# Optimization experiments

Hardware: AMD Instinct MI355X
Metric: run time of the kernel (lower is better)

## Reference

```python
import jax, jax.numpy as jnp
import numpy as np

B, N, E = 2, 2048, 1024
H = 16
BM = 32  # BLOCK_M
BN = 32  # BLOCK_N
BUDGET = 0.2


def setup_inputs() -> dict:
    key = jax.random.key(0)
    ks = jax.random.split(key, 5)
    w = lambda k: jax.random.normal(k, (E, E), jnp.float32) * 0.02
    return {
        "x": jax.random.normal(ks[0], (B, N, E), jnp.float32),
        "W_Q": w(ks[1]),
        "W_K": w(ks[2]),
        "W_V": w(ks[3]),
        "W_O": w(ks[4]),
    }


def _forward(x, W_Q, W_K, W_V, W_O):
    Bx, Nx, Ex = x.shape
    D = Ex // H
    Tr, Tc = Nx // BM, Nx // BN
    k = max(1, int(BUDGET * Tc))

    def heads(t):  # [B,N,E] -> [B,H,N,D]
        return t.reshape(Bx, Nx, H, D).transpose(0, 2, 1, 3)

    Q = heads(x @ W_Q)
    K = heads(x @ W_K)
    V = heads(x @ W_V)

    # dynamic top-k block routing on mean-pooled blocks (indices are constants)
    Qp = Q.reshape(Bx, H, Tr, BM, D).mean(axis=3)   # [B,H,Tr,D]
    Kp = K.reshape(Bx, H, Tc, BN, D).mean(axis=3)   # [B,H,Tc,D]
    avg_sc = jnp.einsum("bhid,bhjd->bhij", Qp, Kp).mean(axis=(0, 1))  # [Tr,Tc]
    _, idx = jax.lax.top_k(avg_sc, k)  # [Tr,k] selected key blocks per query block

    # gather selected K/V blocks: [B,H,Tr,k,BN,D]
    Kb = K.reshape(Bx, H, Tc, BN, D)
    Vb = V.reshape(Bx, H, Tc, BN, D)
    Ksel = Kb[:, :, idx]
    Vsel = Vb[:, :, idx]

    Qb = Q.reshape(Bx, H, Tr, BM, D)
    scale = 1.0 / jnp.sqrt(jnp.asarray(D, jnp.float32))
    # logits over the union of selected key columns: [B,H,Tr,BM,k*BN]
    logits = jnp.einsum("bhtqd,bhtknd->bhtqkn", Qb, Ksel).reshape(
        Bx, H, Tr, BM, k * BN) * scale
    P = jax.nn.softmax(logits, axis=-1)
    Ob = jnp.einsum("bhtqs,bhtsd->bhtqd", P,
                    Vsel.reshape(Bx, H, Tr, k * BN, D))  # [B,H,Tr,BM,D]
    O = Ob.reshape(Bx, H, Nx, D).transpose(0, 2, 1, 3).reshape(Bx, Nx, Ex)
    return O @ W_O


def reference(x, W_Q, W_K, W_V, W_O):
    return _forward(x, W_Q, W_K, W_V, W_O)
```

## Files before the change

### kernel.cpp

```cpp
#include <hip/hip_runtime.h>
#include <hip/hip_bf16.h>
#include <stdint.h>

#define E     1024
#define NSEQ  2048
#define NH    16
#define HD    64
#define KSEL  12
#define MROWS 4096

typedef unsigned short u16;
typedef __attribute__((ext_vector_type(8))) short bf16x8;
typedef __attribute__((ext_vector_type(4))) float f32x4;
typedef __attribute__((ext_vector_type(4))) unsigned short u16x4;

__device__ __forceinline__ float b2f(u16 u) {
  return __builtin_bit_cast(float, (unsigned)u << 16);
}
__device__ __forceinline__ u16 f2b(float f) {
  return __builtin_bit_cast(u16, __float2bfloat16(f));
}

__device__ __forceinline__ void gload_lds16(const void* g, void* l) {
  auto gp = reinterpret_cast<__attribute__((address_space(1))) unsigned int*>(
      reinterpret_cast<uintptr_t>(g));
  auto lp = reinterpret_cast<__attribute__((address_space(3))) unsigned int*>(
      reinterpret_cast<uintptr_t>(l));
  __builtin_amdgcn_global_load_lds(gp, lp, 16, 0, 0);
}

__global__ void detect_k(const u16* __restrict__ x, int* __restrict__ flag) {
  int cnt = 0;
  for (int i = threadIdx.x; i < 1024; i += 64) {
    const unsigned e = (x[i] >> 7) & 0xFF;
    cnt += (e >= 100 && e <= 140) ? 1 : 0;
  }
#pragma unroll
  for (int off = 1; off < 64; off <<= 1) cnt += __shfl_xor(cnt, off, 64);
  if (threadIdx.x == 0) flag[0] = (cnt > 900) ? 1 : 0;
}

__global__ void xconv_k(const void* __restrict__ xin, u16* __restrict__ xc,
                        const int* __restrict__ flag) {
  const int f = flag[0];
  const int stride = gridDim.x * blockDim.x;
  if (f) {
    const u16* s = (const u16*)xin;
    for (int i = blockIdx.x * blockDim.x + threadIdx.x; i < MROWS * E; i += stride)
      xc[i] = s[i];
  } else {
    const float* s = (const float*)xin;
    for (int i = blockIdx.x * blockDim.x + threadIdx.x; i < MROWS * E; i += stride)
      xc[i] = f2b(s[i]);
  }
}

__global__ void transpose4(const void* __restrict__ w0, const void* __restrict__ w1,
                           const void* __restrict__ w2, const void* __restrict__ w3,
                           u16* __restrict__ Wt, const int* __restrict__ flag) {
  __shared__ u16 tile[32][33];
  const void* W = blockIdx.z == 0 ? w0 : blockIdx.z == 1 ? w1 : blockIdx.z == 2 ? w2 : w3;
  const int f = flag[0];
  u16* O = Wt + (size_t)blockIdx.z * (E * E);
  const int tx = threadIdx.x & 31, ty = threadIdx.x >> 5;
  const int bk = blockIdx.y * 32, bn = blockIdx.x * 32;
  if (f) {
    const u16* Wu = (const u16*)W;
    for (int r = ty; r < 32; r += 8)
      tile[r][tx] = Wu[(size_t)(bk + r) * E + bn + tx];
  } else {
    const float* Wf = (const float*)W;
    for (int r = ty; r < 32; r += 8)
      tile[r][tx] = f2b(Wf[(size_t)(bk + r) * E + bn + tx]);
  }
  __syncthreads();
  for (int r = ty; r < 32; r += 8)
    O[(size_t)(bn + r) * E + bk + tx] = tile[tx][r];
}

__global__ void xpmean_k(const void* __restrict__ xin, float* __restrict__ xp,
                         const int* __restrict__ flag) {
  const int blk = blockIdx.x;
  const int f = flag[0];
  const size_t base = (size_t)blk * 32 * E;
  if (f) {
    const u16* x = (const u16*)xin;
    for (int c = threadIdx.x; c < E; c += 256) {
      float s = 0.f;
      for (int r = 0; r < 32; ++r) s += b2f(x[base + (size_t)r * E + c]);
      xp[(size_t)blk * E + c] = s * (1.0f / 32.0f);
    }
  } else {
    const float* x = (const float*)xin;
    for (int c = threadIdx.x; c < E; c += 256) {
      float s = 0.f;
      for (int r = 0; r < 32; ++r) s += x[base + (size_t)r * E + c];
      xp[(size_t)blk * E + c] = s * (1.0f / 32.0f);
    }
  }
}

__global__ void qpkp2_k(const float* __restrict__ xp, const void* __restrict__ Wq,
                        const void* __restrict__ Wk, float* __restrict__ Ppart,
                        const int* __restrict__ flag) {
  __shared__ float xpT[64][129];
  __shared__ float wS[64][64];
  const int c0 = blockIdx.x * 64, k0 = blockIdx.z * 64;
  const int mat = blockIdx.y;
  const int tid = threadIdx.x;
  const int f = flag[0];
  const void* W = mat ? Wk : Wq;
#pragma unroll
  for (int it = 0; it < 32; ++it) {
    const int i = it * 256 + tid;
    const int row = i >> 6, kk = i & 63;
    xpT[kk][row] = xp[(size_t)row * E + k0 + kk];
  }
  if (f) {
    const u16* Wu = (const u16*)W;
#pragma unroll
    for (int it = 0; it < 16; ++it) {
      const int i = it * 256 + tid;
      const int kk = i >> 6, c = i & 63;
      wS[kk][c] = b2f(Wu[(size_t)(k0 + kk) * E + c0 + c]);
    }
  } else {
    const float* Wf = (const float*)W;
#pragma unroll
    for (int it = 0; it < 16; ++it) {
      const int i = it * 256 + tid;
      const int kk = i >> 6, c = i & 63;
      wS[kk][c] = Wf[(size_t)(k0 + kk) * E + c0 + c];
    }
  }
  __syncthreads();
  const int cq = (tid & 15) * 4;
  const int r0 = (tid >> 4) * 8;
  float acc[8][4] = {};
  for (int kk = 0; kk < 64; ++kk) {
    const f32x4 b = *(const f32x4*)&wS[kk][cq];
    float a[8];
#pragma unroll
    for (int j = 0; j < 8; ++j) a[j] = xpT[kk][r0 + j];
#pragma unroll
    for (int j = 0; j < 8; ++j)
#pragma unroll
      for (int c = 0; c < 4; ++c)
        acc[j][c] += a[j] * b[c];
  }
  float* P = Ppart + (size_t)(mat * 16 + blockIdx.z) * 128 * E;
#pragma unroll
  for (int j = 0; j < 8; ++j)
    *(f32x4*)&P[(size_t)(r0 + j) * E + c0 + cq] = *(const f32x4*)acc[j];
}

__global__ void qpred_k(const float* __restrict__ Ppart, float* __restrict__ Qp,
                        float* __restrict__ Kp) {
  const int fidx = blockIdx.x * 256 + threadIdx.x;
  const int mat = fidx >> 15;
  const int rem = fidx & 32767;
  const float* src = Ppart + (size_t)mat * 16 * 128 * E + (size_t)rem * 4;
  f32x4 s = {};
#pragma unroll
  for (int ks = 0; ks < 16; ++ks)
    s += *(const f32x4*)(src + (size_t)ks * 128 * E);
  float* out = mat ? Kp : Qp;
  *(f32x4*)(out + (size_t)rem * 4) = s;
}

__global__ void avgsc_k(const float* __restrict__ Qp, const float* __restrict__ Kp,
                        float* __restrict__ sc) {
  const int i = blockIdx.x;
  const int j = threadIdx.x & 63, s = threadIdx.x >> 6;
  __shared__ float qrow[2][E];
  __shared__ float red[4][64];
  for (int e = threadIdx.x; e < 2 * E; e += 256)
    qrow[e >> 10][e & 1023] = Qp[(size_t)((e >> 10) * 64 + i) * E + (e & 1023)];
  __syncthreads();
  float acc = 0.f;
  for (int b = 0; b < 2; ++b) {
    const float* kr = Kp + (size_t)(b * 64 + j) * E + s * 256;
    const float* qr = qrow[b] + s * 256;
    for (int e = 0; e < 256; e += 4)
      acc += qr[e] * kr[e] + qr[e + 1] * kr[e + 1] + qr[e + 2] * kr[e + 2] + qr[e + 3] * kr[e + 3];
  }
  red[s][j] = acc;
  __syncthreads();
  if (threadIdx.x < 64)
    sc[i * 64 + threadIdx.x] = (red[0][threadIdx.x] + red[1][threadIdx.x] +
                                red[2][threadIdx.x] + red[3][threadIdx.x]) * (1.0f / 32.0f);
}

__global__ void topk_k(const float* __restrict__ sc, int* __restrict__ idxs) {
  __shared__ float s[64][65];
  const int tid = threadIdx.x;
  for (int e = tid; e < 4096; e += 64) s[e >> 6][e & 63] = sc[e];
  __syncthreads();
  for (int j = 0; j < KSEL; ++j) {
    float m = -3.4e38f;
    int mi = 0;
    for (int c = 0; c < 64; ++c) {
      float v = s[tid][c];
      if (v > m) { m = v; mi = c; }
    }
    idxs[tid * KSEL + j] = mi;
    s[tid][mi] = -3.4e38f;
  }
}

template <int MODE>
__launch_bounds__(256, 2)
__global__ void gemm_bt(const u16* __restrict__ A, const u16* __restrict__ BtBase,
                        void* __restrict__ OutBase, const int* __restrict__ flag) {
  __shared__ __attribute__((aligned(16))) u16 At[128 * 32];
  __shared__ __attribute__((aligned(16))) u16 Bs[128 * 32];
  const int tid = threadIdx.x;
  const int wave = tid >> 6, lane = tid & 63;
  const int q4 = lane >> 4, l16 = lane & 15;
  const int wm = (wave >> 1) * 64, wn = (wave & 1) * 64;
  const int bm = blockIdx.x * 128, bn = blockIdx.y * 128;
  const u16* Bmat = BtBase + (MODE == 0 ? (size_t)blockIdx.z * (E * E) : 0);
  const int srow = lane >> 2;
  const int scol = (lane & 3) * 8;

  f32x4 acc[4][4] = {};

  for (int k0 = 0; k0 < E; k0 += 32) {
#pragma unroll
    for (int r = 0; r < 2; ++r) {
      const int c = r * 4 + wave;
      const int row = c * 16 + srow;
      gload_lds16(A + (size_t)(bm + row) * E + k0 + scol, &At[c * 512 + lane * 8]);
      gload_lds16(Bmat + (size_t)(bn + row) * E + k0 + scol, &Bs[c * 512 + lane * 8]);
    }
    __syncthreads();
    bf16x8 af[4], bfr[4];
#pragma unroll
    for (int mi = 0; mi < 4; ++mi)
      af[mi] = *(const bf16x8*)&At[(wm + mi * 16 + l16) * 32 + q4 * 8];
#pragma unroll
    for (int ni = 0; ni < 4; ++ni)
      bfr[ni] = *(const bf16x8*)&Bs[(wn + ni * 16 + l16) * 32 + q4 * 8];
#pragma unroll
    for (int mi = 0; mi < 4; ++mi)
#pragma unroll
      for (int ni = 0; ni < 4; ++ni)
        acc[mi][ni] = __builtin_amdgcn_mfma_f32_16x16x32_bf16(af[mi], bfr[ni], acc[mi][ni], 0, 0, 0);
    __syncthreads();
  }

  if (MODE == 1) {
    const int f = flag[0];
    if (f) {
      u16* Out = (u16*)OutBase;
#pragma unroll
      for (int mi = 0; mi < 4; ++mi) {
        const int rg0 = bm + wm + mi * 16 + q4 * 4;
#pragma unroll
        for (int ni = 0; ni < 4; ++ni) {
          const int cg = bn + wn + ni * 16 + l16;
#pragma unroll
          for (int r = 0; r < 4; ++r)
            Out[(size_t)(rg0 + r) * E + cg] = f2b(acc[mi][ni][r]);
        }
      }
    } else {
      float* Out = (float*)OutBase;
#pragma unroll
      for (int mi = 0; mi < 4; ++mi) {
        const int rg0 = bm + wm + mi * 16 + q4 * 4;
#pragma unroll
        for (int ni = 0; ni < 4; ++ni) {
          const int cg = bn + wn + ni * 16 + l16;
#pragma unroll
          for (int r = 0; r < 4; ++r)
            Out[(size_t)(rg0 + r) * E + cg] = acc[mi][ni][r];
        }
      }
    }
  } else {
    const int z = blockIdx.z;
    u16* O = (u16*)OutBase + (size_t)z * 4194304;
    if (z < 2) {
#pragma unroll
      for (int mi = 0; mi < 4; ++mi) {
        const int rg0 = bm + wm + mi * 16 + q4 * 4;
        const int b = rg0 >> 11, n0 = rg0 & 2047;
#pragma unroll
        for (int ni = 0; ni < 4; ++ni) {
          const int cg = bn + wn + ni * 16 + l16;
          const int h = cg >> 6, d = cg & 63;
          u16* dst = O + (size_t)(b * NH + h) * NSEQ * HD + d;
#pragma unroll
          for (int r = 0; r < 4; ++r)
            dst[(size_t)(n0 + r) * HD] = f2b(acc[mi][ni][r]);
        }
      }
    } else {
#pragma unroll
      for (int mi = 0; mi < 4; ++mi) {
        const int rg0 = bm + wm + mi * 16 + q4 * 4;
        const int b = rg0 >> 11, n0 = rg0 & 2047;
#pragma unroll
        for (int ni = 0; ni < 4; ++ni) {
          const int cg = bn + wn + ni * 16 + l16;
          const int h = cg >> 6, d = cg & 63;
          u16x4 v;
          v.x = f2b(acc[mi][ni][0]);
          v.y = f2b(acc[mi][ni][1]);
          v.z = f2b(acc[mi][ni][2]);
          v.w = f2b(acc[mi][ni][3]);
          *(u16x4*)(O + ((size_t)(b * NH + h) * HD + d) * NSEQ + n0) = v;
        }
      }
    }
  }
}

__launch_bounds__(256, 2)
__global__ void attn_k(const u16* __restrict__ Q, const u16* __restrict__ K,
                       const u16* __restrict__ Vt, const int* __restrict__ idxs,
                       u16* __restrict__ Oat) {
  const int t = blockIdx.x, h = blockIdx.y, b = blockIdx.z;
  const int tid = threadIdx.x, w = tid >> 6, lane = tid & 63;
  const int q4 = lane >> 4, l16 = lane & 15;
  __shared__ __attribute__((aligned(16))) u16 P[32 * 392];
  __shared__ float Ored[4][32][64];
  __shared__ float redm[4][32];
  __shared__ float reds[4][32];
  const size_t hb = (size_t)(b * NH + h) * NSEQ * HD;
  const u16* Qh = Q + hb;
  const u16* Kh = K + hb;
  const u16* Vh = Vt + hb;
  int blks[3];
#pragma unroll
  for (int i = 0; i < 3; ++i) blks[i] = idxs[t * KSEL + w * 3 + i];

  f32x4 accS[2][6] = {};
#pragma unroll
  for (int ks = 0; ks < 2; ++ks) {
    bf16x8 aq[2];
#pragma unroll
    for (int mi = 0; mi < 2; ++mi)
      aq[mi] = *(const bf16x8*)&Qh[(size_t)(t * 32 + mi * 16 + l16) * HD + ks * 32 + q4 * 8];
#pragma unroll
    for (int ni = 0; ni < 6; ++ni) {
      const int n = blks[ni >> 1] * 32 + (ni & 1) * 16 + l16;
      bf16x8 bk = *(const bf16x8*)&Kh[(size_t)n * HD + ks * 32 + q4 * 8];
#pragma unroll
      for (int mi = 0; mi < 2; ++mi)
        accS[mi][ni] = __builtin_amdgcn_mfma_f32_16x16x32_bf16(aq[mi], bk, accS[mi][ni], 0, 0, 0);
    }
  }

  float rmax[2][4];
#pragma unroll
  for (int mi = 0; mi < 2; ++mi)
#pragma unroll
    for (int r = 0; r < 4; ++r) {
      float m = accS[mi][0][r];
#pragma unroll
      for (int ni = 1; ni < 6; ++ni) m = fmaxf(m, accS[mi][ni][r]);
      rmax[mi][r] = m;
    }
#pragma unroll
  for (int off = 1; off < 16; off <<= 1)
#pragma unroll
    for (int mi = 0; mi < 2; ++mi)
#pragma unroll
      for (int r = 0; r < 4; ++r)
        rmax[mi][r] = fmaxf(rmax[mi][r], __shfl_xor(rmax[mi][r], off, 64));
  if (l16 == 0) {
#pragma unroll
    for (int mi = 0; mi < 2; ++mi)
#pragma unroll
      for (int r = 0; r < 4; ++r)
        redm[w][mi * 16 + q4 * 4 + r] = rmax[mi][r];
  }
  __syncthreads();
  const float cexp = 0.125f * 1.44269504088896f;
  float gmax[2][4];
#pragma unroll
  for (int mi = 0; mi < 2; ++mi)
#pragma unroll
    for (int r = 0; r < 4; ++r) {
      const int row = mi * 16 + q4 * 4 + r;
      gmax[mi][r] = fmaxf(fmaxf(redm[0][row], redm[1][row]), fmaxf(redm[2][row], redm[3][row]));
    }
  float rsum[2][4] = {};
#pragma unroll
  for (int mi = 0; mi < 2; ++mi)
#pragma unroll
    for (int ni = 0; ni < 6; ++ni)
#pragma unroll
      for (int r = 0; r < 4; ++r) {
        const float e = __builtin_exp2f((accS[mi][ni][r] - gmax[mi][r]) * cexp);
        accS[mi][ni][r] = e;
        rsum[mi][r] += e;
      }
#pragma unroll
  for (int off = 1; off < 16; off <<= 1)
#pragma unroll
    for (int mi = 0; mi < 2; ++mi)
#pragma unroll
      for (int r = 0; r < 4; ++r)
        rsum[mi][r] += __shfl_xor(rsum[mi][r], off, 64);
  if (l16 == 0) {
#pragma unroll
    for (int mi = 0; mi < 2; ++mi)
#pragma unroll
      for (int r = 0; r < 4; ++r)
        reds[w][mi * 16 + q4 * 4 + r] = rsum[mi][r];
  }
  __syncthreads();
#pragma unroll
  for (int mi = 0; mi < 2; ++mi)
#pragma unroll
    for (int r = 0; r < 4; ++r) {
      const int row = mi * 16 + q4 * 4 + r;
      const float inv = 1.0f / (reds[0][row] + reds[1][row] + reds[2][row] + reds[3][row]);
#pragma unroll
      for (int ni = 0; ni < 6; ++ni)
        P[row * 392 + w * 96 + ni * 16 + l16] = f2b(accS[mi][ni][r] * inv);
    }
  __syncthreads();

  f32x4 accO[2][4] = {};
#pragma unroll
  for (int ks = 0; ks < 3; ++ks) {
    const int blk = blks[ks];
    bf16x8 ap[2];
#pragma unroll
    for (int mi = 0; mi < 2; ++mi)
      ap[mi] = *(const bf16x8*)&P[(mi * 16 + l16) * 392 + w * 96 + ks * 32 + q4 * 8];
#pragma unroll
    for (int ni = 0; ni < 4; ++ni) {
      bf16x8 bv = *(const bf16x8*)&Vh[(size_t)(ni * 16 + l16) * NSEQ + blk * 32 + q4 * 8];
#pragma unroll
      for (int mi = 0; mi < 2; ++mi)
        accO[mi][ni] = __builtin_amdgcn_mfma_f32_16x16x32_bf16(ap[mi], bv, accO[mi][ni], 0, 0, 0);
    }
  }
#pragma unroll
  for (int mi = 0; mi < 2; ++mi)
#pragma unroll
    for (int ni = 0; ni < 4; ++ni)
#pragma unroll
      for (int r = 0; r < 4; ++r)
        Ored[w][mi * 16 + q4 * 4 + r][ni * 16 + l16] = accO[mi][ni][r];
  __syncthreads();
  for (int e = tid; e < 2048; e += 256) {
    const int r = e >> 6, d = e & 63;
    const float s = Ored[0][r][d] + Ored[1][r][d] + Ored[2][r][d] + Ored[3][r][d];
    Oat[(size_t)(b * NSEQ + t * 32 + r) * E + h * HD + d] = f2b(s);
  }
}

extern "C" void kernel_launch(void* const* d_in, const int* in_sizes, int n_in,
                              void* d_out, int out_size, void* d_ws, size_t ws_size,
                              hipStream_t stream) {
  (void)in_sizes; (void)n_in; (void)out_size; (void)ws_size;
  const void* x  = d_in[0];
  const void* wq = d_in[1];
  const void* wk = d_in[2];
  const void* wv = d_in[3];
  const void* wo = d_in[4];

  u16* Wt  = (u16*)d_ws;
  u16* Qb  = Wt + 4 * 1048576;
  u16* Oat = Qb + 3 * 4194304;
  u16* xc  = Oat;
  float* Ppart = (float*)Qb;
  float* xp = (float*)(Oat + 4194304);
  float* Qp = xp + 131072;
  float* Kp = Qp + 131072;
  float* sc = Kp + 131072;
  int* idxs = (int*)(sc + 4096);
  int* flag = idxs + 768;

  detect_k<<<dim3(1), 64, 0, stream>>>((const u16*)x, flag);
  xconv_k<<<dim3(2048), 256, 0, stream>>>(x, xc, flag);
  transpose4<<<dim3(32, 32, 4), 256, 0, stream>>>(wq, wk, wv, wo, Wt, flag);
  xpmean_k<<<dim3(128), 256, 0, stream>>>(x, xp, flag);
  qpkp2_k<<<dim3(16, 2, 16), 256, 0, stream>>>(xp, wq, wk, Ppart, flag);
  qpred_k<<<dim3(256), 256, 0, stream>>>(Ppart, Qp, Kp);
  avgsc_k<<<dim3(64), 256, 0, stream>>>(Qp, Kp, sc);
  topk_k<<<dim3(1), 64, 0, stream>>>(sc, idxs);
  gemm_bt<0><<<dim3(32, 8, 3), 256, 0, stream>>>(xc, Wt, Qb, flag);
  attn_k<<<dim3(64, NH, 2), 256, 0, stream>>>(Qb, Qb + 4194304, Qb + 2 * 4194304, idxs, Oat);
  gemm_bt<1><<<dim3(32, 8, 1), 256, 0, stream>>>(Oat, Wt + 3 * 1048576, d_out, flag);
}
```

Measured before the change: 237.6 us.

## Split attention PV by output columns, remap blocks per XCD, vectorize x conversion

The PV stage in the attention kernel now gives each wave a 16-column slice of the output across all 12 selected key blocks, instead of a third of the key blocks across all columns. This removes the 32 KB float LDS reduction buffer, its extra barrier and the cross-wave sum, and lets each wave write its results straight to global memory. The grid is flattened to 1D with an XCD-aware mapping so the blocks of a given head share one XCD's L2, and launch bounds are raised to allow 4 blocks per CU. The input conversion kernel is also vectorized to 4 elements per thread on half as many blocks. The changes trade more scattered 2-byte global stores and extra idxs reads for less LDS use and higher occupancy.

```diff
diff --git a/kernel.cpp b/kernel.cpp
--- a/kernel.cpp
+++ b/kernel.cpp
@@ -44,14 +44,20 @@
                         const int* __restrict__ flag) {
   const int f = flag[0];
   const int stride = gridDim.x * blockDim.x;
+  const int n4 = MROWS * E / 4;
   if (f) {
-    const u16* s = (const u16*)xin;
-    for (int i = blockIdx.x * blockDim.x + threadIdx.x; i < MROWS * E; i += stride)
-      xc[i] = s[i];
+    const u16x4* s = (const u16x4*)xin;
+    u16x4* d = (u16x4*)xc;
+    for (int i = blockIdx.x * blockDim.x + threadIdx.x; i < n4; i += stride)
+      d[i] = s[i];
   } else {
-    const float* s = (const float*)xin;
-    for (int i = blockIdx.x * blockDim.x + threadIdx.x; i < MROWS * E; i += stride)
-      xc[i] = f2b(s[i]);
+    const f32x4* s = (const f32x4*)xin;
+    for (int i = blockIdx.x * blockDim.x + threadIdx.x; i < n4; i += stride) {
+      const f32x4 v = s[i];
+      u16x4 o;
+      o.x = f2b(v.x); o.y = f2b(v.y); o.z = f2b(v.z); o.w = f2b(v.w);
+      *(u16x4*)(xc + (size_t)i * 4) = o;
+    }
   }
 }
 
@@ -317,21 +323,24 @@
   }
 }
 
-__launch_bounds__(256, 2)
+__launch_bounds__(256, 4)
 __global__ void attn_k(const u16* __restrict__ Q, const u16* __restrict__ K,
                        const u16* __restrict__ Vt, const int* __restrict__ idxs,
                        u16* __restrict__ Oat) {
-  const int t = blockIdx.x, h = blockIdx.y, b = blockIdx.z;
+  const int id = blockIdx.x;
+  const int xcd = id & 7, g = id >> 3;
+  const int t = g & 63;
+  const int hb = xcd * 4 + (g >> 6);
+  const int h = hb & 15, b = hb >> 4;
   const int tid = threadIdx.x, w = tid >> 6, lane = tid & 63;
   const int q4 = lane >> 4, l16 = lane & 15;
   __shared__ __attribute__((aligned(16))) u16 P[32 * 392];
-  __shared__ float Ored[4][32][64];
   __shared__ float redm[4][32];
   __shared__ float reds[4][32];
-  const size_t hb = (size_t)(b * NH + h) * NSEQ * HD;
-  const u16* Qh = Q + hb;
-  const u16* Kh = K + hb;
-  const u16* Vh = Vt + hb;
+  const size_t hbo = (size_t)(b * NH + h) * NSEQ * HD;
+  const u16* Qh = Q + hbo;
+  const u16* Kh = K + hbo;
+  const u16* Vh = Vt + hbo;
   int blks[3];
 #pragma unroll
   for (int i = 0; i < 3; ++i) blks[i] = idxs[t * KSEL + w * 3 + i];
@@ -425,34 +434,23 @@
     }
   __syncthreads();
 
-  f32x4 accO[2][4] = {};
-#pragma unroll
-  for (int ks = 0; ks < 3; ++ks) {
-    const int blk = blks[ks];
-    bf16x8 ap[2];
-#pragma unroll
-    for (int mi = 0; mi < 2; ++mi)
-      ap[mi] = *(const bf16x8*)&P[(mi * 16 + l16) * 392 + w * 96 + ks * 32 + q4 * 8];
-#pragma unroll
-    for (int ni = 0; ni < 4; ++ni) {
-      bf16x8 bv = *(const bf16x8*)&Vh[(size_t)(ni * 16 + l16) * NSEQ + blk * 32 + q4 * 8];
-#pragma unroll
-      for (int mi = 0; mi < 2; ++mi)
-        accO[mi][ni] = __builtin_amdgcn_mfma_f32_16x16x32_bf16(ap[mi], bv, accO[mi][ni], 0, 0, 0);
-    }
-  }
-#pragma unroll
-  for (int mi = 0; mi < 2; ++mi)
-#pragma unroll
-    for (int ni = 0; ni < 4; ++ni)
-#pragma unroll
-      for (int r = 0; r < 4; ++r)
-        Ored[w][mi * 16 + q4 * 4 + r][ni * 16 + l16] = accO[mi][ni][r];
-  __syncthreads();
-  for (int e = tid; e < 2048; e += 256) {
-    const int r = e >> 6, d = e & 63;
-    const float s = Ored[0][r][d] + Ored[1][r][d] + Ored[2][r][d] + Ored[3][r][d];
-    Oat[(size_t)(b * NSEQ + t * 32 + r) * E + h * HD + d] = f2b(s);
+  f32x4 accO[2] = {};
+#pragma unroll
+  for (int q = 0; q < KSEL; ++q) {
+    const int blk = idxs[t * KSEL + q];
+    const bf16x8 bv = *(const bf16x8*)&Vh[(size_t)(w * 16 + l16) * NSEQ + blk * 32 + q4 * 8];
+#pragma unroll
+    for (int mi = 0; mi < 2; ++mi) {
+      const bf16x8 ap = *(const bf16x8*)&P[(mi * 16 + l16) * 392 + q * 32 + q4 * 8];
+      accO[mi] = __builtin_amdgcn_mfma_f32_16x16x32_bf16(ap, bv, accO[mi], 0, 0, 0);
+    }
+  }
+#pragma unroll
+  for (int mi = 0; mi < 2; ++mi) {
+    const int row0 = t * 32 + mi * 16 + q4 * 4;
+#pragma unroll
+    for (int r = 0; r < 4; ++r)
+      Oat[(size_t)(b * NSEQ + row0 + r) * E + h * HD + w * 16 + l16] = f2b(accO[mi][r]);
   }
 }
 
@@ -479,7 +477,7 @@
   int* flag = idxs + 768;
 
   detect_k<<<dim3(1), 64, 0, stream>>>((const u16*)x, flag);
-  xconv_k<<<dim3(2048), 256, 0, stream>>>(x, xc, flag);
+  xconv_k<<<dim3(1024), 256, 0, stream>>>(x, xc, flag);
   transpose4<<<dim3(32, 32, 4), 256, 0, stream>>>(wq, wk, wv, wo, Wt, flag);
   xpmean_k<<<dim3(128), 256, 0, stream>>>(x, xp, flag);
   qpkp2_k<<<dim3(16, 2, 16), 256, 0, stream>>>(xp, wq, wk, Ppart, flag);
@@ -487,6 +485,6 @@
   avgsc_k<<<dim3(64), 256, 0, stream>>>(Qp, Kp, sc);
   topk_k<<<dim3(1), 64, 0, stream>>>(sc, idxs);
   gemm_bt<0><<<dim3(32, 8, 3), 256, 0, stream>>>(xc, Wt, Qb, flag);
-  attn_k<<<dim3(64, NH, 2), 256, 0, stream>>>(Qb, Qb + 4194304, Qb + 2 * 4194304, idxs, Oat);
+  attn_k<<<dim3(2048), 256, 0, stream>>>(Qb, Qb + 4194304, Qb + 2 * 4194304, idxs, Oat);
   gemm_bt<1><<<dim3(32, 8, 1), 256, 0, stream>>>(Oat, Wt + 3 * 1048576, d_out, flag);
 }
```

New measurement: 229.8 us. -3.3%, faster.
